# Optimization experiments

Hardware: AMD Instinct MI355X
Metric: run time of the kernel (lower is better)

## Reference

```python
import jax, jax.numpy as jnp
import numpy as np

N, K, M = 1024, 256, 1024
INIT_SCALE = 0.1


def setup_inputs() -> dict:
    key = jax.random.key(0)
    kx, kw = jax.random.split(key)
    x = jax.random.normal(kx, (N, K), dtype=jnp.float32)
    weight = jax.random.normal(kw, (M, K), dtype=jnp.float32) * INIT_SCALE
    return {"x": x, "weight": weight}


def reference(x, weight):
    # Tropical (max-plus) matmul: out[n, m] = max_k(|x[n, k]| + |w[m, k]|)
    ax = jnp.abs(x)        # [N, K]
    aw = jnp.abs(weight)   # [M, K]
    # broadcast to [N, M, K] then reduce over K (mirrors the original expand+add+max)
    return jnp.max(ax[:, None, :] + aw[None, :, :], axis=2)  # [N, M]
```

## Files before the change

kernel.cpp:

```cpp
#include <hip/hip_runtime.h>


typedef float v2f __attribute__((ext_vector_type(2)));
typedef float v4f __attribute__((ext_vector_type(4)));

constexpr int TILE = 64;
constexpr int KB   = 64;
constexpr int KKP  = KB / 2;
constexpr int PITCH = TILE + 2;

static __device__ inline v2f mk2(float a, float b) { v2f r; r.x = a; r.y = b; return r; }

__global__ void __launch_bounds__(256)
tropical_kernel(const float* __restrict__ xg, const float* __restrict__ wg,
                float* __restrict__ outg)
{
    constexpr int K = 256;
    constexpr int M = 1024;

    __shared__ __align__(16) v2f xs[KKP * PITCH];
    __shared__ __align__(16) v2f ws[KKP * PITCH];

    const int tid = threadIdx.x;
    const int tx = tid & 15;
    const int ty = tid >> 4;
    const int bn = (int)(blockIdx.x >> 4) * TILE;
    const int bm = (int)(blockIdx.x & 15) * TILE;

    const float* xbase = xg + (bn + ty) * K + 4 * tx;
    const float* wbase = wg + (bm + ty) * K + 4 * tx;

    v4f xr[4], wr[4];
#pragma unroll
    for (int i = 0; i < 4; ++i) {
        xr[i] = *(const v4f*)(xbase + (16 * i) * K);
        wr[i] = *(const v4f*)(wbase + (16 * i) * K);
    }

    float acc[4][4];
#pragma unroll
    for (int i = 0; i < 4; ++i)
#pragma unroll
        for (int j = 0; j < 4; ++j) acc[i][j] = 0.0f;

    for (int chunk = 0; chunk < K / KB; ++chunk) {
        __syncthreads();
#pragma unroll
        for (int i = 0; i < 4; ++i) {
            v4f fx = xr[i], fw = wr[i];
            int n = ty + 16 * i;
            xs[(2 * tx)     * PITCH + n] = mk2(fabsf(fx.x), fabsf(fx.y));
            xs[(2 * tx + 1) * PITCH + n] = mk2(fabsf(fx.z), fabsf(fx.w));
            ws[(2 * tx)     * PITCH + n] = mk2(fabsf(fw.x), fabsf(fw.y));
            ws[(2 * tx + 1) * PITCH + n] = mk2(fabsf(fw.z), fabsf(fw.w));
        }
        __syncthreads();

        if (chunk + 1 < K / KB) {
            const float* xn = xbase + (chunk + 1) * KB;
            const float* wn = wbase + (chunk + 1) * KB;
#pragma unroll
            for (int i = 0; i < 4; ++i) {
                xr[i] = *(const v4f*)(xn + (16 * i) * K);
                wr[i] = *(const v4f*)(wn + (16 * i) * K);
            }
        }

#pragma unroll
        for (int kk = 0; kk < KKP; ++kk) {
            const v2f* xrow = &xs[kk * PITCH + 4 * ty];
            const v2f* wrow = &ws[kk * PITCH + 4 * tx];
            v4f xa = *(const v4f*)xrow;
            v4f xb = *(const v4f*)(xrow + 2);
            v4f wa = *(const v4f*)wrow;
            v4f wb = *(const v4f*)(wrow + 2);

            v2f xp[4] = { mk2(xa.x, xa.y), mk2(xa.z, xa.w),
                          mk2(xb.x, xb.y), mk2(xb.z, xb.w) };
            v2f wp[4] = { mk2(wa.x, wa.y), mk2(wa.z, wa.w),
                          mk2(wb.x, wb.y), mk2(wb.z, wb.w) };
#pragma unroll
            for (int i = 0; i < 4; ++i)
#pragma unroll
                for (int j = 0; j < 4; ++j) {
                    v2f s = xp[i] + wp[j];
                    acc[i][j] = fmaxf(acc[i][j], fmaxf(s.x, s.y));
                }
        }
    }

#pragma unroll
    for (int i = 0; i < 4; ++i) {
        v4f o; o.x = acc[i][0]; o.y = acc[i][1]; o.z = acc[i][2]; o.w = acc[i][3];
        *(v4f*)(outg + (bn + 4 * ty + i) * M + bm + 4 * tx) = o;
    }
}

extern "C" void kernel_launch(void* const* d_in, const int* in_sizes, int n_in,
                              void* d_out, int out_size, void* d_ws, size_t ws_size,
                              hipStream_t stream)
{
    const float* x = (const float*)d_in[0];
    const float* w = (const float*)d_in[1];
    float* out = (float*)d_out;

    dim3 grid(256);
    dim3 block(256);
    tropical_kernel<<<grid, block, 0, stream>>>(x, w, out);
}
```

Baseline: 74.80 us.

## Shrink block tile to 32x32 with 2x2 per-thread outputs and 1024 blocks

Halves the output tile per block from 64x64 to 32x32 and each thread now computes a 2x2 block of outputs instead of 4x4, launching 1024 blocks rather than 256. The aim is to fill all CUs of the MI355X (256 CUs) with more waves and cut per-thread register use. The cost is lower arithmetic intensity: each LDS v4f load now feeds 4 outputs instead of 16, so LDS traffic per output rises and global reloads of x and w double.

```diff
diff --git a/kernel.cpp b/kernel.cpp
--- a/kernel.cpp
+++ b/kernel.cpp
@@ -4,12 +4,10 @@
 typedef float v2f __attribute__((ext_vector_type(2)));
 typedef float v4f __attribute__((ext_vector_type(4)));
 
-constexpr int TILE = 64;
-constexpr int KB   = 64;
-constexpr int KKP  = KB / 2;
+constexpr int TILE  = 32;
+constexpr int KB    = 64;
+constexpr int KKP   = KB / 2;
 constexpr int PITCH = TILE + 2;
-
-static __device__ inline v2f mk2(float a, float b) { v2f r; r.x = a; r.y = b; return r; }
 
 __global__ void __launch_bounds__(256)
 tropical_kernel(const float* __restrict__ xg, const float* __restrict__ wg,
@@ -24,76 +22,62 @@
     const int tid = threadIdx.x;
     const int tx = tid & 15;
     const int ty = tid >> 4;
-    const int bn = (int)(blockIdx.x >> 4) * TILE;
-    const int bm = (int)(blockIdx.x & 15) * TILE;
+    const int bn = (int)(blockIdx.x >> 5) * TILE;
+    const int bm = (int)(blockIdx.x & 31) * TILE;
 
-    const float* xbase = xg + (bn + ty) * K + 4 * tx;
-    const float* wbase = wg + (bm + ty) * K + 4 * tx;
+    const int r = tid >> 3;
+    const int c = (tid & 7) * 8;
+    const float* xbase = xg + (bn + r) * K + c;
+    const float* wbase = wg + (bm + r) * K + c;
 
-    v4f xr[4], wr[4];
-#pragma unroll
-    for (int i = 0; i < 4; ++i) {
-        xr[i] = *(const v4f*)(xbase + (16 * i) * K);
-        wr[i] = *(const v4f*)(wbase + (16 * i) * K);
-    }
+    v4f xr0 = *(const v4f*)(xbase);
+    v4f xr1 = *(const v4f*)(xbase + 4);
+    v4f wr0 = *(const v4f*)(wbase);
+    v4f wr1 = *(const v4f*)(wbase + 4);
 
-    float acc[4][4];
-#pragma unroll
-    for (int i = 0; i < 4; ++i)
-#pragma unroll
-        for (int j = 0; j < 4; ++j) acc[i][j] = 0.0f;
+    float a00 = 0.f, a01 = 0.f, a10 = 0.f, a11 = 0.f;
+
+    const int kp = c >> 1;
 
     for (int chunk = 0; chunk < K / KB; ++chunk) {
         __syncthreads();
-#pragma unroll
-        for (int i = 0; i < 4; ++i) {
-            v4f fx = xr[i], fw = wr[i];
-            int n = ty + 16 * i;
-            xs[(2 * tx)     * PITCH + n] = mk2(fabsf(fx.x), fabsf(fx.y));
-            xs[(2 * tx + 1) * PITCH + n] = mk2(fabsf(fx.z), fabsf(fx.w));
-            ws[(2 * tx)     * PITCH + n] = mk2(fabsf(fw.x), fabsf(fw.y));
-            ws[(2 * tx + 1) * PITCH + n] = mk2(fabsf(fw.z), fabsf(fw.w));
-        }
+        xs[(kp + 0) * PITCH + r] = (v2f){fabsf(xr0.x), fabsf(xr0.y)};
+        xs[(kp + 1) * PITCH + r] = (v2f){fabsf(xr0.z), fabsf(xr0.w)};
+        xs[(kp + 2) * PITCH + r] = (v2f){fabsf(xr1.x), fabsf(xr1.y)};
+        xs[(kp + 3) * PITCH + r] = (v2f){fabsf(xr1.z), fabsf(xr1.w)};
+        ws[(kp + 0) * PITCH + r] = (v2f){fabsf(wr0.x), fabsf(wr0.y)};
+        ws[(kp + 1) * PITCH + r] = (v2f){fabsf(wr0.z), fabsf(wr0.w)};
+        ws[(kp + 2) * PITCH + r] = (v2f){fabsf(wr1.x), fabsf(wr1.y)};
+        ws[(kp + 3) * PITCH + r] = (v2f){fabsf(wr1.z), fabsf(wr1.w)};
         __syncthreads();
 
         if (chunk + 1 < K / KB) {
             const float* xn = xbase + (chunk + 1) * KB;
             const float* wn = wbase + (chunk + 1) * KB;
-#pragma unroll
-            for (int i = 0; i < 4; ++i) {
-                xr[i] = *(const v4f*)(xn + (16 * i) * K);
-                wr[i] = *(const v4f*)(wn + (16 * i) * K);
-            }
+            xr0 = *(const v4f*)(xn);
+            xr1 = *(const v4f*)(xn + 4);
+            wr0 = *(const v4f*)(wn);
+            wr1 = *(const v4f*)(wn + 4);
         }
 
 #pragma unroll
         for (int kk = 0; kk < KKP; ++kk) {
-            const v2f* xrow = &xs[kk * PITCH + 4 * ty];
-            const v2f* wrow = &ws[kk * PITCH + 4 * tx];
-            v4f xa = *(const v4f*)xrow;
-            v4f xb = *(const v4f*)(xrow + 2);
-            v4f wa = *(const v4f*)wrow;
-            v4f wb = *(const v4f*)(wrow + 2);
-
-            v2f xp[4] = { mk2(xa.x, xa.y), mk2(xa.z, xa.w),
-                          mk2(xb.x, xb.y), mk2(xb.z, xb.w) };
-            v2f wp[4] = { mk2(wa.x, wa.y), mk2(wa.z, wa.w),
-                          mk2(wb.x, wb.y), mk2(wb.z, wb.w) };
-#pragma unroll
-            for (int i = 0; i < 4; ++i)
-#pragma unroll
-                for (int j = 0; j < 4; ++j) {
-                    v2f s = xp[i] + wp[j];
-                    acc[i][j] = fmaxf(acc[i][j], fmaxf(s.x, s.y));
-                }
+            v4f xv = *(const v4f*)&xs[kk * PITCH + 2 * ty];
+            v4f wv = *(const v4f*)&ws[kk * PITCH + 2 * tx];
+            v2f x0 = {xv.x, xv.y}, x1 = {xv.z, xv.w};
+            v2f w0 = {wv.x, wv.y}, w1 = {wv.z, wv.w};
+            v2f s;
+            s = x0 + w0; a00 = fmaxf(a00, fmaxf(s.x, s.y));
+            s = x0 + w1; a01 = fmaxf(a01, fmaxf(s.x, s.y));
+            s = x1 + w0; a10 = fmaxf(a10, fmaxf(s.x, s.y));
+            s = x1 + w1; a11 = fmaxf(a11, fmaxf(s.x, s.y));
         }
     }
 
-#pragma unroll
-    for (int i = 0; i < 4; ++i) {
-        v4f o; o.x = acc[i][0]; o.y = acc[i][1]; o.z = acc[i][2]; o.w = acc[i][3];
-        *(v4f*)(outg + (bn + 4 * ty + i) * M + bm + 4 * tx) = o;
-    }
+    const int n0 = bn + 2 * ty;
+    const int m0 = bm + 2 * tx;
+    *(v2f*)(outg + n0 * M + m0)       = (v2f){a00, a01};
+    *(v2f*)(outg + (n0 + 1) * M + m0) = (v2f){a10, a11};
 }
 
 extern "C" void kernel_launch(void* const* d_in, const int* in_sizes, int n_in,
@@ -104,7 +88,7 @@
     const float* w = (const float*)d_in[1];
     float* out = (float*)d_out;
 
-    dim3 grid(256);
+    dim3 grid(1024);
     dim3 block(256);
     tropical_kernel<<<grid, block, 0, stream>>>(x, w, out);
 }
```

Result: faster. 70.86 us (-5.3%).
